# Kernel tuning notes

Measured on AMD Instinct MI355X. Metric: run time of the kernel, lower is better.

## Reference

```python
import jax, jax.numpy as jnp
import numpy as np

B, D, H, NS = 64, 2048, 4096, 25  # batch, x_dim (num_links), n_hidden=2*x_dim, n_steps


def setup_inputs() -> dict:
    key = jax.random.key(0)
    ks = jax.random.split(key, 12)
    # binary half-masks per leapfrog step (faithful to _construct_masks with np_seed=1)
    rng = np.random.RandomState(1)
    masks = np.zeros((NS, D), np.float32)
    for i in range(NS):
        idx = rng.permutation(D)[: D // 2]
        masks[i, idx] = 1.0
    # sinusoidal time encoding per step (_construct_time)
    ts = np.stack([
        [np.cos(2 * np.pi * i / NS), np.sin(2 * np.pi * i / NS)] for i in range(NS)
    ]).astype(np.float32)

    def lin(k, shape, fan_in):
        return jax.random.normal(k, shape, jnp.float32) / np.sqrt(fan_in)

    return dict(
        position=jax.random.normal(ks[0], (B, D), jnp.float32),
        momentum_f=jax.random.normal(ks[1], (B, D), jnp.float32),
        momentum_b=jax.random.normal(ks[2], (B, D), jnp.float32),
        u_dir=jax.random.uniform(ks[3], (B,), jnp.float32),
        u_accept=jax.random.uniform(ks[4], (B,), jnp.float32),
        eps=jnp.full((1,), 0.1, jnp.float32),
        masks=jnp.asarray(masks),
        ts=jnp.asarray(ts),
        # stacked params for the two GenericNets: [0]=position_fn, [1]=momentum_fn
        W1=lin(ks[5], (2, D, H), D), W2=lin(ks[6], (2, D, H), D),
        Wt=lin(ks[7], (2, 2, H), 2), b1=jnp.zeros((2, H), jnp.float32),
        Wh=lin(ks[8], (2, H, H), H), bh=jnp.zeros((2, H), jnp.float32),
        Ws=lin(ks[9], (2, H, D), H), bs=jnp.zeros((2, D), jnp.float32),
        cs=jnp.zeros((2, D), jnp.float32),
        Wtr=lin(ks[10], (2, H, D), H), btr=jnp.zeros((2, D), jnp.float32),
        Wq=lin(ks[11], (2, H, D), H), bq=jnp.zeros((2, D), jnp.float32),
        cq=jnp.zeros((2, D), jnp.float32),
    )


def reference(position, momentum_f, momentum_b, u_dir, u_accept, eps, masks, ts,
              W1, W2, Wt, b1, Wh, bh, Ws, bs, cs, Wtr, btr, Wq, bq, cq):
    e = eps[0]
    POS, MOM = 0, 1

    def net(n, a, b, t):
        # GenericNet: two-hidden-layer MLP emitting (scale S, translation T, transformation Q)
        h = jax.nn.relu(a @ W1[n] + b @ W2[n] + t @ Wt[n] + b1[n])
        h = jax.nn.relu(h @ Wh[n] + bh[n])
        S = jnp.tanh(h @ Ws[n] + bs[n]) * jnp.exp(cs[n])
        T = h @ Wtr[n] + btr[n]
        Q = jnp.tanh(h @ Wq[n] + bq[n]) * jnp.exp(cq[n])
        return S, T, Q

    def potential(x):              # U(1) gauge-style action: sum(1 - cos(x))
        return jnp.sum(1.0 - jnp.cos(x), axis=1)

    def grad_potential(x):
        return jnp.sin(x)

    def hamiltonian(x, v):
        return potential(x) + 0.5 * jnp.sum(v * v, axis=1)

    def mom_fwd(pos, mom, t):
        g = grad_potential(pos)
        S, T, Q = net(MOM, pos, g, t)
        sc, tr = 0.5 * e * S, e * Q
        mom = mom * jnp.exp(sc) - 0.5 * e * (jnp.exp(tr) * g - T)
        return mom, jnp.sum(sc, axis=1)

    def pos_fwd(pos, mom, t, m, minv):
        S, T, Q = net(POS, mom, m * pos, t)
        sc, tr = e * S, e * Q
        pos = m * pos + minv * (pos * jnp.exp(sc) + e * (jnp.exp(tr) * mom + T))
        return pos, jnp.sum(minv * sc, axis=1)

    def mom_bwd(pos, mom, t):
        g = grad_potential(pos)
        S, T, Q = net(MOM, pos, g, t)
        sc, tr = -0.5 * e * S, e * Q
        mom = jnp.exp(sc) * (mom + 0.5 * e * (jnp.exp(tr) * g - T))
        return mom, jnp.sum(sc, axis=1)

    def pos_bwd(pos, mom, t, m, minv):
        S, T, Q = net(POS, mom, m * pos, t)
        sc, tr = e * S, e * Q
        pos = m * pos + minv * jnp.exp(sc) * (pos - e * (jnp.exp(tr) * mom + T))
        return pos, jnp.sum(minv * sc, axis=1)

    def step_fwd(carry, xs):
        pos, mom, sld = carry
        m, t = xs
        t = t[None, :]
        minv = 1.0 - m
        mom, ld = mom_fwd(pos, mom, t); sld = sld + ld
        pos, ld = pos_fwd(pos, mom, t, m, minv); sld = sld + ld
        pos, ld = pos_fwd(pos, mom, t, minv, m); sld = sld + ld
        mom, ld = mom_fwd(pos, mom, t); sld = sld + ld
        return (pos, mom, sld), None

    def step_bwd(carry, xs):
        pos, mom, sld = carry
        m, t = xs
        t = t[None, :]
        minv = 1.0 - m
        mom, ld = mom_bwd(pos, mom, t); sld = sld + ld
        pos, ld = pos_bwd(pos, mom, t, minv, m); sld = sld + ld
        pos, ld = pos_bwd(pos, mom, t, m, minv); sld = sld + ld
        mom, ld = mom_bwd(pos, mom, t); sld = sld + ld
        return (pos, mom, sld), None

    zero = jnp.zeros(position.shape[0], position.dtype)
    (pf, mf, sldf), _ = jax.lax.scan(step_fwd, (position, momentum_f, zero), (masks, ts))
    (pb, mb, sldb), _ = jax.lax.scan(step_bwd, (position, momentum_b, zero), (masks[::-1], ts[::-1]))

    def accept_prob(mom0, pos1, mom1, sld):
        d = hamiltonian(position, mom0) - hamiltonian(pos1, mom1) + sld
        p = jnp.exp(jnp.minimum(d, 0.0))
        return jnp.where(jnp.isfinite(p), p, jnp.zeros_like(p))

    apf = accept_prob(momentum_f, pf, mf, sldf)
    apb = accept_prob(momentum_b, pb, mb, sldb)

    fmask = (u_dir > 0.5).astype(position.dtype)
    bmask = 1.0 - fmask
    position_post = fmask[:, None] * pf + bmask[:, None] * pb
    momentum_post = fmask[:, None] * mf + bmask[:, None] * mb
    ap = fmask * apf + bmask * apb
    amask = (ap > u_accept).astype(position.dtype)
    position_out = amask[:, None] * position_post + (1.0 - amask)[:, None] * position
    return position_post, momentum_post, ap, position_out
```

## Files before the change

kernel.cpp:

```cpp
#include <hip/hip_runtime.h>

#define BD   64
#define DD   2048
#define HH   4096
#define NSS  25
#define BBr  128

typedef _Float16 halfx8 __attribute__((ext_vector_type(8)));
typedef float    floatx4 __attribute__((ext_vector_type(4)));

__device__ __forceinline__ unsigned short f2h_bits(float x) {
    union { _Float16 h; unsigned short u; } c;
    c.h = (_Float16)x;
    return c.u;
}

__global__ void init_kernel(const float* __restrict__ position,
                            const float* __restrict__ momf,
                            const float* __restrict__ momb,
                            float* __restrict__ pos, float* __restrict__ mom,
                            float* __restrict__ sld,
                            unsigned short* __restrict__ Abuf) {
    int idx = blockIdx.x * 256 + threadIdx.x;
    int r = idx >> 11, d = idx & 2047;
    float p = position[((r & 63) << 11) + d];
    pos[idx] = p;
    mom[idx] = (r < 64) ? momf[(r << 11) + d] : momb[((r - 64) << 11) + d];
    Abuf[(r << 12) + d]        = f2h_bits(p);
    Abuf[(r << 12) + 2048 + d] = f2h_bits(sinf(p));
    if (idx < BBr) sld[idx] = 0.f;
}

__global__ __launch_bounds__(256) void transpose_cvt_kernel(
        const float* __restrict__ src, int ldi,
        unsigned short* __restrict__ dst, int ldo) {
    __shared__ float tile[32][33];
    const int rb = blockIdx.y * 32;
    const int cb = blockIdx.x * 32;
    const int t  = threadIdx.x;
    const int r  = t >> 3;
    const int c4 = (t & 7) * 4;
    float4 v = *reinterpret_cast<const float4*>(src + (size_t)(rb + r) * ldi + cb + c4);
    tile[r][c4 + 0] = v.x; tile[r][c4 + 1] = v.y;
    tile[r][c4 + 2] = v.z; tile[r][c4 + 3] = v.w;
    __syncthreads();
    union { unsigned short us[4]; uint2 v; } pk;
#pragma unroll
    for (int j = 0; j < 4; ++j) pk.us[j] = f2h_bits(tile[c4 + j][r]);
    *reinterpret_cast<uint2*>(dst + (size_t)(cb + r) * ldo + rb + c4) = pk.v;
}

template <int EPI, int KS>
__global__ __launch_bounds__(KS * 256, 4) void gemm_bt_kernel(
        const unsigned short* __restrict__ A, int lda, int K,
        const unsigned short* __restrict__ BT,
        void* __restrict__ Cout, int ldc,
        const float* __restrict__ biasp, const float* __restrict__ Wtn,
        const float* __restrict__ ts, int sF, int sB) {
    const int tid  = threadIdx.x;
    const int lane = tid & 63;
    const int mw   = (tid >> 6) & 3;
    const int kq   = tid >> 8;
    const int fl   = lane & 15;
    const int qd   = lane >> 4;
    const int bn   = blockIdx.x * 16;

    const int Kq = K / KS;
    const unsigned short* pa0 = A + (size_t)(mw * 32 + fl) * lda + kq * Kq + qd * 8;
    const unsigned short* pa1 = pa0 + (size_t)16 * lda;
    const unsigned short* pb  = BT + (size_t)(bn + fl) * K + kq * Kq + qd * 8;

    floatx4 acc0 = {0.f, 0.f, 0.f, 0.f};
    floatx4 acc1 = {0.f, 0.f, 0.f, 0.f};

    for (int k0 = 0; k0 < Kq; k0 += 128) {
#pragma unroll
        for (int u = 0; u < 4; ++u) {
            halfx8 a0 = *reinterpret_cast<const halfx8*>(pa0 + u * 32);
            halfx8 a1 = *reinterpret_cast<const halfx8*>(pa1 + u * 32);
            halfx8 b  = *reinterpret_cast<const halfx8*>(pb  + u * 32);
            acc0 = __builtin_amdgcn_mfma_f32_16x16x32_f16(a0, b, acc0, 0, 0, 0);
            acc1 = __builtin_amdgcn_mfma_f32_16x16x32_f16(a1, b, acc1, 0, 0, 0);
        }
        pa0 += 128; pa1 += 128; pb += 128;
    }

    __shared__ float red[(KS - 1) * 4][64][8];
    if (kq > 0) {
        float* p = &red[(kq - 1) * 4 + mw][lane][0];
#pragma unroll
        for (int j = 0; j < 4; ++j) { p[j] = acc0[j]; p[j + 4] = acc1[j]; }
    }
    __syncthreads();
    if (kq != 0) return;
#pragma unroll
    for (int q = 0; q < KS - 1; ++q) {
        const float* p = &red[q * 4 + mw][lane][0];
#pragma unroll
        for (int j = 0; j < 4; ++j) { acc0[j] += p[j]; acc1[j] += p[j + 4]; }
    }

    const int col = bn + fl;
#pragma unroll
    for (int fn = 0; fn < 2; ++fn) {
        floatx4 a = (fn == 0) ? acc0 : acc1;
        const int row_base = mw * 32 + fn * 16 + qd * 4;
#pragma unroll
        for (int rr = 0; rr < 4; ++rr) {
            int row = row_base + rr;
            float v = a[rr];
            if (EPI == 0) {
                int sidx = (row < 64) ? sF : sB;
                v += biasp[col] + ts[2 * sidx] * Wtn[col] + ts[2 * sidx + 1] * Wtn[HH + col];
                v = fmaxf(v, 0.f);
                ((unsigned short*)Cout)[(size_t)row * ldc + col] = f2h_bits(v);
            } else if (EPI == 1) {
                v = fmaxf(v + biasp[col], 0.f);
                ((unsigned short*)Cout)[(size_t)row * ldc + col] = f2h_bits(v);
            } else {
                ((float*)Cout)[(size_t)row * ldc + col] = v;
            }
        }
    }
}

template <int BMODE, int EPI>
__global__ __launch_bounds__(256) void gemm_kernel(
        const unsigned short* __restrict__ A, int lda, int K,
        const float* __restrict__ Bp0, const float* __restrict__ Bp1,
        const float* __restrict__ Bp2, int ldb,
        void* __restrict__ Cout, int ldc,
        const float* __restrict__ biasp, const float* __restrict__ Wtn,
        const float* __restrict__ ts, int sF, int sB) {
    __shared__ unsigned short As[32][40];
    __shared__ unsigned short Bs[64][40];

    const int tid  = threadIdx.x;
    const int wave = tid >> 6;
    const int lane = tid & 63;
    const int fl   = lane & 15;
    const int qd   = lane >> 4;
    const int bm   = blockIdx.y * 32;
    const int bn   = blockIdx.x * 64;
    const int wm   = (wave >> 1) * 16;
    const int wn   = (wave & 1) * 32;

    const int ar = tid >> 3;
    const int ak = (tid & 7) * 4;
    const int kloc = wave * 8;
    const int bnl  = lane;

    floatx4 acc0 = {0.f, 0.f, 0.f, 0.f};
    floatx4 acc1 = {0.f, 0.f, 0.f, 0.f};

    for (int k0 = 0; k0 < K; k0 += 32) {
        *reinterpret_cast<uint2*>(&As[ar][ak]) =
            *reinterpret_cast<const uint2*>(A + (size_t)(bm + ar) * lda + k0 + ak);

        float fv[8];
        if (BMODE == 0) {
            int kk = k0 + kloc;
            const float* base = (kk < 2048) ? (Bp0 + (size_t)kk * ldb)
                                            : (Bp1 + (size_t)(kk - 2048) * ldb);
            base += bn + bnl;
#pragma unroll
            for (int j = 0; j < 8; ++j) fv[j] = base[(size_t)j * ldb];
        } else if (BMODE == 1) {
            const float* base = Bp0 + (size_t)(k0 + kloc) * ldb + bn + bnl;
#pragma unroll
            for (int j = 0; j < 8; ++j) fv[j] = base[(size_t)j * ldb];
        } else {
            int third = bn >> 11;
            const float* Bsel = (third == 0) ? Bp0 : ((third == 1) ? Bp1 : Bp2);
            const float* base = Bsel + (size_t)(k0 + kloc) * ldb + (bn - (third << 11)) + bnl;
#pragma unroll
            for (int j = 0; j < 8; ++j) fv[j] = base[(size_t)j * ldb];
        }
        union { unsigned short us[8]; uint4 v; } pk;
#pragma unroll
        for (int j = 0; j < 8; ++j) pk.us[j] = f2h_bits(fv[j]);
        *reinterpret_cast<uint4*>(&Bs[bnl][kloc]) = pk.v;

        __syncthreads();

        halfx8 afr = *reinterpret_cast<const halfx8*>(&As[wm + fl][qd * 8]);
        halfx8 bf0 = *reinterpret_cast<const halfx8*>(&Bs[wn + fl][qd * 8]);
        halfx8 bf1 = *reinterpret_cast<const halfx8*>(&Bs[wn + 16 + fl][qd * 8]);
        acc0 = __builtin_amdgcn_mfma_f32_16x16x32_f16(afr, bf0, acc0, 0, 0, 0);
        acc1 = __builtin_amdgcn_mfma_f32_16x16x32_f16(afr, bf1, acc1, 0, 0, 0);

        __syncthreads();
    }

    const int row0 = bm + wm + qd * 4;
#pragma unroll
    for (int fn = 0; fn < 2; ++fn) {
        floatx4 a = (fn == 0) ? acc0 : acc1;
        int col = bn + wn + fn * 16 + fl;
#pragma unroll
        for (int rr = 0; rr < 4; ++rr) {
            int row = row0 + rr;
            float v = a[rr];
            if (EPI == 0) {
                int sidx = (row < 64) ? sF : sB;
                v += biasp[col] + ts[2 * sidx] * Wtn[col] + ts[2 * sidx + 1] * Wtn[HH + col];
                v = fmaxf(v, 0.f);
                ((unsigned short*)Cout)[(size_t)row * ldc + col] = f2h_bits(v);
            } else if (EPI == 1) {
                v = fmaxf(v + biasp[col], 0.f);
                ((unsigned short*)Cout)[(size_t)row * ldc + col] = f2h_bits(v);
            } else {
                ((float*)Cout)[(size_t)row * ldc + col] = v;
            }
        }
    }
}

__device__ __forceinline__ void block_reduce_atomic(float v, float* dst) {
    for (int off = 32; off; off >>= 1) v += __shfl_down(v, off, 64);
    __shared__ float red[4];
    if ((threadIdx.x & 63) == 0) red[threadIdx.x >> 6] = v;
    __syncthreads();
    if (threadIdx.x == 0) atomicAdd(dst, red[0] + red[1] + red[2] + red[3]);
}

__global__ void update_mom_kernel(const float* __restrict__ pos, float* __restrict__ mom,
                                  float* __restrict__ sld, const float* __restrict__ STQ,
                                  const float* __restrict__ bs, const float* __restrict__ cs,
                                  const float* __restrict__ btr, const float* __restrict__ bq,
                                  const float* __restrict__ cq, const float* __restrict__ eps,
                                  const float* __restrict__ masks, int sF, int sB,
                                  int writeNext, unsigned short* __restrict__ Abuf) {
    int r = blockIdx.y;
    int d = blockIdx.x * 256 + threadIdx.x;
    float e = eps[0];
    size_t ro = (size_t)r * 6144;
    float S = tanhf(STQ[ro + d] + bs[d]) * expf(cs[d]);
    float T = STQ[ro + 2048 + d] + btr[d];
    float Q = tanhf(STQ[ro + 4096 + d] + bq[d]) * expf(cq[d]);
    size_t idx = (size_t)r * 2048 + d;
    float p = pos[idx], v = mom[idx];
    float g = sinf(p);
    float tr = e * Q, sc;
    if (r < 64) { sc = 0.5f * e * S;  v = v * expf(sc) - 0.5f * e * (expf(tr) * g - T); }
    else        { sc = -0.5f * e * S; v = expf(sc) * (v + 0.5f * e * (expf(tr) * g - T)); }
    mom[idx] = v;
    if (writeNext) {
        float m2 = (r < 64) ? masks[sF * 2048 + d] : 1.f - masks[sB * 2048 + d];
        Abuf[(r << 12) + d]        = f2h_bits(v);
        Abuf[(r << 12) + 2048 + d] = f2h_bits(m2 * p);
    }
    block_reduce_atomic(sc, sld + r);
}

__global__ void update_pos_kernel(float* __restrict__ pos, const float* __restrict__ mom,
                                  float* __restrict__ sld, const float* __restrict__ STQ,
                                  const float* __restrict__ bs, const float* __restrict__ cs,
                                  const float* __restrict__ btr, const float* __restrict__ bq,
                                  const float* __restrict__ cq, const float* __restrict__ eps,
                                  const float* __restrict__ masks, int sF, int sB, int sub,
                                  unsigned short* __restrict__ Abuf) {
    int r = blockIdx.y;
    int d = blockIdx.x * 256 + threadIdx.x;
    float e = eps[0];
    size_t ro = (size_t)r * 6144;
    float S = tanhf(STQ[ro + d] + bs[d]) * expf(cs[d]);
    float T = STQ[ro + 2048 + d] + btr[d];
    float Q = tanhf(STQ[ro + 4096 + d] + bq[d]) * expf(cq[d]);
    size_t idx = (size_t)r * 2048 + d;
    float p = pos[idx], v = mom[idx];
    float sc = e * S, tr = e * Q;
    float mf = masks[sF * 2048 + d], mb = masks[sB * 2048 + d];
    float pn, ld;
    if (r < 64) {
        float m  = (sub == 2) ? mf : 1.f - mf;
        float mi = 1.f - m;
        pn = m * p + mi * (p * expf(sc) + e * (expf(tr) * v + T));
        ld = mi * sc;
    } else {
        float m  = (sub == 2) ? 1.f - mb : mb;
        float mi = 1.f - m;
        pn = m * p + mi * expf(sc) * (p - e * (expf(tr) * v + T));
        ld = mi * sc;
    }
    pos[idx] = pn;
    if (sub == 2) {
        float m3 = (r < 64) ? 1.f - mf : mb;
        Abuf[(r << 12) + d]        = f2h_bits(v);
        Abuf[(r << 12) + 2048 + d] = f2h_bits(m3 * pn);
    } else {
        Abuf[(r << 12) + d]        = f2h_bits(pn);
        Abuf[(r << 12) + 2048 + d] = f2h_bits(sinf(pn));
    }
    block_reduce_atomic(ld, sld + r);
}

__global__ void accept_kernel(const float* __restrict__ position,
                              const float* __restrict__ momf, const float* __restrict__ momb,
                              const float* __restrict__ pos, const float* __restrict__ mom,
                              const float* __restrict__ sld, float* __restrict__ ap_all) {
    int r = blockIdx.x;
    int rb = r & 63;
    const float* m0 = (r < 64) ? (momf + (size_t)rb * 2048) : (momb + (size_t)rb * 2048);
    float s = 0.f;
    for (int d = threadIdx.x; d < 2048; d += 256) {
        float x0 = position[rb * 2048 + d];
        float v0 = m0[d];
        float x1 = pos[(size_t)r * 2048 + d];
        float v1 = mom[(size_t)r * 2048 + d];
        s += (cosf(x1) - cosf(x0)) + 0.5f * (v0 * v0 - v1 * v1);
    }
    for (int off = 32; off; off >>= 1) s += __shfl_down(s, off, 64);
    __shared__ float red[4];
    if ((threadIdx.x & 63) == 0) red[threadIdx.x >> 6] = s;
    __syncthreads();
    if (threadIdx.x == 0) {
        float dd = red[0] + red[1] + red[2] + red[3] + sld[r];
        float p = isnan(dd) ? 0.f : expf(dd < 0.f ? dd : 0.f);
        if (!isfinite(p)) p = 0.f;
        ap_all[r] = p;
    }
}

__global__ void combine_kernel(const float* __restrict__ position,
                               const float* __restrict__ u_dir, const float* __restrict__ u_accept,
                               const float* __restrict__ pos, const float* __restrict__ mom,
                               const float* __restrict__ ap_all, float* __restrict__ out) {
    int idx = blockIdx.x * 256 + threadIdx.x;
    int b = idx >> 11, d = idx & 2047;
    float fm = (u_dir[b] > 0.5f) ? 1.f : 0.f;
    float pf = pos[(size_t)b * 2048 + d],       pb = pos[(size_t)(64 + b) * 2048 + d];
    float mf = mom[(size_t)b * 2048 + d],       mb = mom[(size_t)(64 + b) * 2048 + d];
    float ppost = fm * pf + (1.f - fm) * pb;
    float mpost = fm * mf + (1.f - fm) * mb;
    float ap = fm * ap_all[b] + (1.f - fm) * ap_all[64 + b];
    float am = (ap > u_accept[b]) ? 1.f : 0.f;
    out[idx] = ppost;
    out[131072 + idx] = mpost;
    if (d == 0) out[262144 + b] = ap;
    out[262208 + idx] = am * ppost + (1.f - am) * position[idx];
}

extern "C" void kernel_launch(void* const* d_in, const int* in_sizes, int n_in,
                              void* d_out, int out_size, void* d_ws, size_t ws_size,
                              hipStream_t stream) {
    const float* position   = (const float*)d_in[0];
    const float* momentum_f = (const float*)d_in[1];
    const float* momentum_b = (const float*)d_in[2];
    const float* u_dir      = (const float*)d_in[3];
    const float* u_accept   = (const float*)d_in[4];
    const float* eps        = (const float*)d_in[5];
    const float* masks      = (const float*)d_in[6];
    const float* ts         = (const float*)d_in[7];
    const float* W1         = (const float*)d_in[8];
    const float* W2         = (const float*)d_in[9];
    const float* Wt         = (const float*)d_in[10];
    const float* b1         = (const float*)d_in[11];
    const float* Wh         = (const float*)d_in[12];
    const float* bh         = (const float*)d_in[13];
    const float* Ws         = (const float*)d_in[14];
    const float* bs         = (const float*)d_in[15];
    const float* cs         = (const float*)d_in[16];
    const float* Wtr        = (const float*)d_in[17];
    const float* btr        = (const float*)d_in[18];
    const float* Wq         = (const float*)d_in[19];
    const float* bq         = (const float*)d_in[20];
    const float* cq         = (const float*)d_in[21];
    float* out = (float*)d_out;

    float* pos    = (float*)d_ws;
    float* mom    = pos + BBr * DD;
    float* sld    = mom + BBr * DD;
    float* ap_all = sld + BBr;
    float* STQ    = ap_all + BBr;
    unsigned short* Abuf = (unsigned short*)(STQ + BBr * 3 * DD);
    unsigned short* h1   = Abuf + (size_t)BBr * 2 * DD;
    unsigned short* h2   = h1 + (size_t)BBr * HH;
    unsigned short* BTw  = h2 + (size_t)BBr * HH;

    const size_t BT1sz = (size_t)HH * 2 * DD;
    const size_t BThsz = (size_t)HH * HH;
    const size_t BT3sz = (size_t)3 * DD * HH;
    const size_t perNet = BT1sz + BThsz + BT3sz;
    unsigned short* BT1[2] = { BTw,                 BTw + perNet };
    unsigned short* BTh[2] = { BTw + BT1sz,         BTw + perNet + BT1sz };
    unsigned short* BT3[2] = { BTw + BT1sz + BThsz, BTw + perNet + BT1sz + BThsz };

    const size_t NEED = (size_t)((char*)(BTw + 2 * perNet) - (char*)d_ws);
    const bool fast = (ws_size >= NEED);

    const size_t DH  = (size_t)DD * HH;
    const size_t HH2 = (size_t)HH * HH;

    init_kernel<<<BBr * DD / 256, 256, 0, stream>>>(position, momentum_f, momentum_b,
                                                    pos, mom, sld, Abuf);

    if (fast) {
        for (int n = 0; n < 2; ++n) {
            transpose_cvt_kernel<<<dim3(HH / 32, DD / 32), 256, 0, stream>>>(
                W1 + n * DH, HH, BT1[n], 2 * DD);
            transpose_cvt_kernel<<<dim3(HH / 32, DD / 32), 256, 0, stream>>>(
                W2 + n * DH, HH, BT1[n] + DD, 2 * DD);
            transpose_cvt_kernel<<<dim3(HH / 32, HH / 32), 256, 0, stream>>>(
                Wh + n * HH2, HH, BTh[n], HH);
            transpose_cvt_kernel<<<dim3(DD / 32, HH / 32), 256, 0, stream>>>(
                Ws + n * DH, DD, BT3[n], HH);
            transpose_cvt_kernel<<<dim3(DD / 32, HH / 32), 256, 0, stream>>>(
                Wtr + n * DH, DD, BT3[n] + (size_t)DD * HH, HH);
            transpose_cvt_kernel<<<dim3(DD / 32, HH / 32), 256, 0, stream>>>(
                Wq + n * DH, DD, BT3[n] + (size_t)2 * DD * HH, HH);
        }
    }

    for (int i = 0; i < NSS; ++i) {
        int sF = i, sB = NSS - 1 - i;
        for (int subidx = 0; subidx < 4; ++subidx) {
            bool isMom = (subidx == 0 || subidx == 3);
            int n = isMom ? 1 : 0;
            int sub = (subidx == 1) ? 2 : 3;

            if (fast) {
                gemm_bt_kernel<0, 4><<<HH / 16, 1024, 0, stream>>>(
                    Abuf, 2 * DD, 2 * DD, BT1[n], h1, HH,
                    b1 + n * HH, Wt + n * 2 * HH, ts, sF, sB);
                gemm_bt_kernel<1, 4><<<HH / 16, 1024, 0, stream>>>(
                    h1, HH, HH, BTh[n], h2, HH,
                    bh + n * HH, nullptr, ts, sF, sB);
                gemm_bt_kernel<2, 2><<<3 * DD / 16, 512, 0, stream>>>(
                    h2, HH, HH, BT3[n], STQ, 3 * DD,
                    nullptr, nullptr, ts, sF, sB);
            } else {
                gemm_kernel<0, 0><<<dim3(HH / 64, 4), 256, 0, stream>>>(
                    Abuf, 2 * DD, 2 * DD,
                    W1 + n * DH, W2 + n * DH, nullptr, HH, h1, HH,
                    b1 + n * HH, Wt + n * 2 * HH, ts, sF, sB);
                gemm_kernel<1, 1><<<dim3(HH / 64, 4), 256, 0, stream>>>(
                    h1, HH, HH, Wh + n * HH2, nullptr, nullptr, HH, h2, HH,
                    bh + n * HH, nullptr, ts, sF, sB);
                gemm_kernel<2, 2><<<dim3(3 * DD / 64, 4), 256, 0, stream>>>(
                    h2, HH, HH, Ws + n * DH, Wtr + n * DH, Wq + n * DH, DD, STQ, 3 * DD,
                    nullptr, nullptr, ts, sF, sB);
            }

            if (isMom)
                update_mom_kernel<<<dim3(DD / 256, BBr), 256, 0, stream>>>(
                    pos, mom, sld, STQ, bs + DD, cs + DD, btr + DD, bq + DD, cq + DD,
                    eps, masks, sF, sB, (subidx == 0) ? 1 : 0, Abuf);
            else
                update_pos_kernel<<<dim3(DD / 256, BBr), 256, 0, stream>>>(
                    pos, mom, sld, STQ, bs, cs, btr, bq, cq, eps, masks, sF, sB, sub, Abuf);
        }
    }

    accept_kernel<<<BBr, 256, 0, stream>>>(position, momentum_f, momentum_b,
                                           pos, mom, sld, ap_all);
    combine_kernel<<<BD * DD / 256, 256, 0, stream>>>(position, u_dir, u_accept,
                                                      pos, mom, ap_all, out);
}
```

Baseline: 18.79 ms.

## Fuse all leapfrog steps into one cooperative persistent kernel with grid syncs

Replaces the roughly 400 separate GEMM and update kernel launches with a single cooperative kernel of 256 blocks. The blocks walk all 25 steps and 4 substeps and use grid.sync between the three GEMM phases and the elementwise update. This removes launch overhead and inter-kernel gaps. The risk is that grid-wide barriers cost time, that 256 blocks of 1024 threads may need to be co-resident, and that the grid is fixed at 256 blocks rather than 4096/16 or 6144/16, so blocks below 128 do the third GEMM twice and load is uneven.

```diff
diff --git a/kernel.cpp b/kernel.cpp
--- a/kernel.cpp
+++ b/kernel.cpp
@@ -1,4 +1,7 @@
 #include <hip/hip_runtime.h>
+#include <hip/hip_cooperative_groups.h>
+
+namespace cg = cooperative_groups;
 
 #define BD   64
 #define DD   2048
@@ -48,6 +51,188 @@
 #pragma unroll
     for (int j = 0; j < 4; ++j) pk.us[j] = f2h_bits(tile[c4 + j][r]);
     *reinterpret_cast<uint2*>(dst + (size_t)(cb + r) * ldo + rb + c4) = pk.v;
+}
+
+__device__ __forceinline__ void gemm_phase(
+        const unsigned short* __restrict__ A, int lda, int K,
+        const unsigned short* __restrict__ BT,
+        void* __restrict__ Cout, int ldc,
+        const float* __restrict__ biasp, const float* __restrict__ Wtn,
+        const float* __restrict__ ts, int sF, int sB,
+        int epi, int bn, float (*red)[64][8]) {
+    const int tid  = threadIdx.x;
+    const int lane = tid & 63;
+    const int mw   = (tid >> 6) & 3;
+    const int kq   = tid >> 8;
+    const int fl   = lane & 15;
+    const int qd   = lane >> 4;
+
+    const int Kq = K >> 2;
+    const unsigned short* pa0 = A + (size_t)(mw * 32 + fl) * lda + kq * Kq + qd * 8;
+    const unsigned short* pa1 = pa0 + (size_t)16 * lda;
+    const unsigned short* pb  = BT + (size_t)(bn + fl) * K + kq * Kq + qd * 8;
+
+    floatx4 acc0 = {0.f, 0.f, 0.f, 0.f};
+    floatx4 acc1 = {0.f, 0.f, 0.f, 0.f};
+
+    for (int k0 = 0; k0 < Kq; k0 += 128) {
+#pragma unroll
+        for (int u = 0; u < 4; ++u) {
+            halfx8 a0 = *reinterpret_cast<const halfx8*>(pa0 + u * 32);
+            halfx8 a1 = *reinterpret_cast<const halfx8*>(pa1 + u * 32);
+            halfx8 b  = *reinterpret_cast<const halfx8*>(pb  + u * 32);
+            acc0 = __builtin_amdgcn_mfma_f32_16x16x32_f16(a0, b, acc0, 0, 0, 0);
+            acc1 = __builtin_amdgcn_mfma_f32_16x16x32_f16(a1, b, acc1, 0, 0, 0);
+        }
+        pa0 += 128; pa1 += 128; pb += 128;
+    }
+
+    if (kq > 0) {
+        float* p = &red[(kq - 1) * 4 + mw][lane][0];
+#pragma unroll
+        for (int j = 0; j < 4; ++j) { p[j] = acc0[j]; p[j + 4] = acc1[j]; }
+    }
+    __syncthreads();
+    if (kq == 0) {
+#pragma unroll
+        for (int q = 0; q < 3; ++q) {
+            const float* p = &red[q * 4 + mw][lane][0];
+#pragma unroll
+            for (int j = 0; j < 4; ++j) { acc0[j] += p[j]; acc1[j] += p[j + 4]; }
+        }
+        const int col = bn + fl;
+#pragma unroll
+        for (int fn = 0; fn < 2; ++fn) {
+            floatx4 a = (fn == 0) ? acc0 : acc1;
+            const int row_base = mw * 32 + fn * 16 + qd * 4;
+#pragma unroll
+            for (int rr = 0; rr < 4; ++rr) {
+                int row = row_base + rr;
+                float v = a[rr];
+                if (epi == 0) {
+                    int sidx = (row < 64) ? sF : sB;
+                    v += biasp[col] + ts[2 * sidx] * Wtn[col] + ts[2 * sidx + 1] * Wtn[HH + col];
+                    v = fmaxf(v, 0.f);
+                    ((unsigned short*)Cout)[(size_t)row * ldc + col] = f2h_bits(v);
+                } else if (epi == 1) {
+                    v = fmaxf(v + biasp[col], 0.f);
+                    ((unsigned short*)Cout)[(size_t)row * ldc + col] = f2h_bits(v);
+                } else {
+                    ((float*)Cout)[(size_t)row * ldc + col] = v;
+                }
+            }
+        }
+    }
+    __syncthreads();
+}
+
+struct PKArgs {
+    const unsigned short *BT1a, *BT1b, *BTha, *BThb, *BT3a, *BT3b;
+    unsigned short *Abuf, *h1, *h2;
+    float *STQ, *pos, *mom, *sld;
+    const float *b1, *bh, *Wt, *ts;
+    const float *bs, *cs, *btr, *bq, *cq, *eps, *masks;
+};
+
+__global__ __launch_bounds__(1024, 4) void persistent_kernel(PKArgs a) {
+    cg::grid_group grid = cg::this_grid();
+    __shared__ float red[12][64][8];
+    __shared__ float redf[16];
+
+    const int tid = threadIdx.x;
+    const int bid = blockIdx.x;
+
+    for (int i = 0; i < NSS; ++i) {
+        const int sF = i, sB = NSS - 1 - i;
+        for (int subidx = 0; subidx < 4; ++subidx) {
+            const bool isMom = (subidx == 0 || subidx == 3);
+            const int sub = (subidx == 1) ? 2 : 3;
+            const unsigned short* B1 = isMom ? a.BT1b : a.BT1a;
+            const unsigned short* Bh = isMom ? a.BThb : a.BTha;
+            const unsigned short* B3 = isMom ? a.BT3b : a.BT3a;
+            const int n = isMom ? 1 : 0;
+
+            gemm_phase(a.Abuf, 2 * DD, 2 * DD, B1, a.h1, HH,
+                       a.b1 + n * HH, a.Wt + n * 2 * HH, a.ts, sF, sB,
+                       0, bid * 16, red);
+            __threadfence(); grid.sync(); __threadfence();
+
+            gemm_phase(a.h1, HH, HH, Bh, a.h2, HH,
+                       a.bh + n * HH, nullptr, a.ts, sF, sB,
+                       1, bid * 16, red);
+            __threadfence(); grid.sync(); __threadfence();
+
+            gemm_phase(a.h2, HH, HH, B3, a.STQ, 3 * DD,
+                       nullptr, nullptr, a.ts, sF, sB, 2, bid * 16, red);
+            if (bid < 128)
+                gemm_phase(a.h2, HH, HH, B3, a.STQ, 3 * DD,
+                           nullptr, nullptr, a.ts, sF, sB, 2, (256 + bid) * 16, red);
+            __threadfence(); grid.sync(); __threadfence();
+
+            {
+                const int r = bid >> 1;
+                const int d = ((bid & 1) << 10) + tid;
+                const float e = a.eps[0];
+                const int off = isMom ? DD : 0;
+                const size_t ro = (size_t)r * 6144;
+                float S = tanhf(a.STQ[ro + d] + a.bs[off + d]) * expf(a.cs[off + d]);
+                float T = a.STQ[ro + 2048 + d] + a.btr[off + d];
+                float Q = tanhf(a.STQ[ro + 4096 + d] + a.bq[off + d]) * expf(a.cq[off + d]);
+                const size_t idx = (size_t)r * 2048 + d;
+                float ld;
+                if (isMom) {
+                    float p = a.pos[idx], v = a.mom[idx];
+                    float g = sinf(p);
+                    float tr = e * Q, sc;
+                    if (r < 64) { sc = 0.5f * e * S;  v = v * expf(sc) - 0.5f * e * (expf(tr) * g - T); }
+                    else        { sc = -0.5f * e * S; v = expf(sc) * (v + 0.5f * e * (expf(tr) * g - T)); }
+                    a.mom[idx] = v;
+                    if (subidx == 0) {
+                        float m2 = (r < 64) ? a.masks[sF * 2048 + d] : 1.f - a.masks[sB * 2048 + d];
+                        a.Abuf[(r << 12) + d]        = f2h_bits(v);
+                        a.Abuf[(r << 12) + 2048 + d] = f2h_bits(m2 * p);
+                    }
+                    ld = sc;
+                } else {
+                    float p = a.pos[idx], v = a.mom[idx];
+                    float sc = e * S, tr = e * Q;
+                    float mf = a.masks[sF * 2048 + d], mb = a.masks[sB * 2048 + d];
+                    float pn;
+                    if (r < 64) {
+                        float m  = (sub == 2) ? mf : 1.f - mf;
+                        float mi = 1.f - m;
+                        pn = m * p + mi * (p * expf(sc) + e * (expf(tr) * v + T));
+                        ld = mi * sc;
+                    } else {
+                        float m  = (sub == 2) ? 1.f - mb : mb;
+                        float mi = 1.f - m;
+                        pn = m * p + mi * expf(sc) * (p - e * (expf(tr) * v + T));
+                        ld = mi * sc;
+                    }
+                    a.pos[idx] = pn;
+                    if (sub == 2) {
+                        float m3 = (r < 64) ? 1.f - mf : mb;
+                        a.Abuf[(r << 12) + d]        = f2h_bits(v);
+                        a.Abuf[(r << 12) + 2048 + d] = f2h_bits(m3 * pn);
+                    } else {
+                        a.Abuf[(r << 12) + d]        = f2h_bits(pn);
+                        a.Abuf[(r << 12) + 2048 + d] = f2h_bits(sinf(pn));
+                    }
+                }
+                for (int o = 32; o; o >>= 1) ld += __shfl_down(ld, o, 64);
+                if ((tid & 63) == 0) redf[tid >> 6] = ld;
+                __syncthreads();
+                if (tid == 0) {
+                    float s = 0.f;
+#pragma unroll
+                    for (int wv = 0; wv < 16; ++wv) s += redf[wv];
+                    atomicAdd(a.sld + r, s);
+                }
+                __syncthreads();
+            }
+            __threadfence(); grid.sync(); __threadfence();
+        }
+    }
 }
 
 template <int EPI, int KS>
@@ -412,43 +597,67 @@
         }
     }
 
-    for (int i = 0; i < NSS; ++i) {
-        int sF = i, sB = NSS - 1 - i;
-        for (int subidx = 0; subidx < 4; ++subidx) {
-            bool isMom = (subidx == 0 || subidx == 3);
-            int n = isMom ? 1 : 0;
-            int sub = (subidx == 1) ? 2 : 3;
-
-            if (fast) {
-                gemm_bt_kernel<0, 4><<<HH / 16, 1024, 0, stream>>>(
-                    Abuf, 2 * DD, 2 * DD, BT1[n], h1, HH,
-                    b1 + n * HH, Wt + n * 2 * HH, ts, sF, sB);
-                gemm_bt_kernel<1, 4><<<HH / 16, 1024, 0, stream>>>(
-                    h1, HH, HH, BTh[n], h2, HH,
-                    bh + n * HH, nullptr, ts, sF, sB);
-                gemm_bt_kernel<2, 2><<<3 * DD / 16, 512, 0, stream>>>(
-                    h2, HH, HH, BT3[n], STQ, 3 * DD,
-                    nullptr, nullptr, ts, sF, sB);
-            } else {
-                gemm_kernel<0, 0><<<dim3(HH / 64, 4), 256, 0, stream>>>(
-                    Abuf, 2 * DD, 2 * DD,
-                    W1 + n * DH, W2 + n * DH, nullptr, HH, h1, HH,
-                    b1 + n * HH, Wt + n * 2 * HH, ts, sF, sB);
-                gemm_kernel<1, 1><<<dim3(HH / 64, 4), 256, 0, stream>>>(
-                    h1, HH, HH, Wh + n * HH2, nullptr, nullptr, HH, h2, HH,
-                    bh + n * HH, nullptr, ts, sF, sB);
-                gemm_kernel<2, 2><<<dim3(3 * DD / 64, 4), 256, 0, stream>>>(
-                    h2, HH, HH, Ws + n * DH, Wtr + n * DH, Wq + n * DH, DD, STQ, 3 * DD,
-                    nullptr, nullptr, ts, sF, sB);
+    bool coopDone = false;
+    if (fast) {
+        int nb = 0;
+        hipError_t occErr = hipOccupancyMaxActiveBlocksPerMultiprocessor(
+            &nb, persistent_kernel, 1024, 0);
+        if (occErr == hipSuccess && nb >= 1) {
+            PKArgs a;
+            a.BT1a = BT1[0]; a.BT1b = BT1[1];
+            a.BTha = BTh[0]; a.BThb = BTh[1];
+            a.BT3a = BT3[0]; a.BT3b = BT3[1];
+            a.Abuf = Abuf; a.h1 = h1; a.h2 = h2;
+            a.STQ = STQ; a.pos = pos; a.mom = mom; a.sld = sld;
+            a.b1 = b1; a.bh = bh; a.Wt = Wt; a.ts = ts;
+            a.bs = bs; a.cs = cs; a.btr = btr; a.bq = bq; a.cq = cq;
+            a.eps = eps; a.masks = masks;
+            void* kargs[] = { &a };
+            hipError_t ce = hipLaunchCooperativeKernel(
+                (const void*)persistent_kernel, dim3(256), dim3(1024), kargs, 0, stream);
+            coopDone = (ce == hipSuccess);
+        }
+    }
+
+    if (!coopDone) {
+        for (int i = 0; i < NSS; ++i) {
+            int sF = i, sB = NSS - 1 - i;
+            for (int subidx = 0; subidx < 4; ++subidx) {
+                bool isMom = (subidx == 0 || subidx == 3);
+                int n = isMom ? 1 : 0;
+                int sub = (subidx == 1) ? 2 : 3;
+
+                if (fast) {
+                    gemm_bt_kernel<0, 4><<<HH / 16, 1024, 0, stream>>>(
+                        Abuf, 2 * DD, 2 * DD, BT1[n], h1, HH,
+                        b1 + n * HH, Wt + n * 2 * HH, ts, sF, sB);
+                    gemm_bt_kernel<1, 4><<<HH / 16, 1024, 0, stream>>>(
+                        h1, HH, HH, BTh[n], h2, HH,
+                        bh + n * HH, nullptr, ts, sF, sB);
+                    gemm_bt_kernel<2, 2><<<3 * DD / 16, 512, 0, stream>>>(
+                        h2, HH, HH, BT3[n], STQ, 3 * DD,
+                        nullptr, nullptr, ts, sF, sB);
+                } else {
+                    gemm_kernel<0, 0><<<dim3(HH / 64, 4), 256, 0, stream>>>(
+                        Abuf, 2 * DD, 2 * DD,
+                        W1 + n * DH, W2 + n * DH, nullptr, HH, h1, HH,
+                        b1 + n * HH, Wt + n * 2 * HH, ts, sF, sB);
+                    gemm_kernel<1, 1><<<dim3(HH / 64, 4), 256, 0, stream>>>(
+                        h1, HH, HH, Wh + n * HH2, nullptr, nullptr, HH, h2, HH,
+                        bh + n * HH, nullptr, ts, sF, sB);
+                    gemm_kernel<2, 2><<<dim3(3 * DD / 64, 4), 256, 0, stream>>>(
+                        h2, HH, HH, Ws + n * DH, Wtr + n * DH, Wq + n * DH, DD, STQ, 3 * DD,
+                        nullptr, nullptr, ts, sF, sB);
+                }
+
+                if (isMom)
+                    update_mom_kernel<<<dim3(DD / 256, BBr), 256, 0, stream>>>(
+                        pos, mom, sld, STQ, bs + DD, cs + DD, btr + DD, bq + DD, cq + DD,
+                        eps, masks, sF, sB, (subidx == 0) ? 1 : 0, Abuf);
+                else
+                    update_pos_kernel<<<dim3(DD / 256, BBr), 256, 0, stream>>>(
+                        pos, mom, sld, STQ, bs, cs, btr, bq, cq, eps, masks, sF, sB, sub, Abuf);
             }
-
-            if (isMom)
-                update_mom_kernel<<<dim3(DD / 256, BBr), 256, 0, stream>>>(
-                    pos, mom, sld, STQ, bs + DD, cs + DD, btr + DD, bq + DD, cq + DD,
-                    eps, masks, sF, sB, (subidx == 0) ? 1 : 0, Abuf);
-            else
-                update_pos_kernel<<<dim3(DD / 256, BBr), 256, 0, stream>>>(
-                    pos, mom, sld, STQ, bs, cs, btr, bq, cq, eps, masks, sF, sB, sub, Abuf);
         }
     }
 
```

Result: no change. 18.77 ms (-0.1%).
